# Kernel optimization log

Measured on AMD Instinct MI355X. Metric: run time of the kernel, lower is better.

The kernel has to match this reference:

```python
import jax, jax.numpy as jnp
import numpy as np

HEAD_DIM = 1024
SCALE = HEAD_DIM ** -0.25  # qk_scale defaults to exponent -0.25


def setup_inputs() -> dict:
    key = jax.random.key(0)
    ks = jax.random.split(key, 6)
    B_s, B_q, C = 4096, 4096, 1024
    return {
        "query": jax.random.normal(ks[0], (B_q, C), dtype=jnp.float32),
        "s": jax.random.normal(ks[1], (B_s, C), dtype=jnp.float32),
        "TG_prompt": jax.random.normal(ks[2], (B_s, C), dtype=jnp.float32),
        "W_qkv": jax.random.normal(ks[3], (3 * HEAD_DIM, C), dtype=jnp.float32) * (C ** -0.5),
        "W_proj_s": jax.random.normal(ks[4], (HEAD_DIM, HEAD_DIM), dtype=jnp.float32) * (HEAD_DIM ** -0.5),
        "W_proj_q": jax.random.normal(ks[5], (HEAD_DIM, HEAD_DIM), dtype=jnp.float32) * (HEAD_DIM ** -0.5),
    }


def reference(query, s, TG_prompt, W_qkv, W_proj_s, W_proj_q):
    B_s = s.shape[0]
    t = s + TG_prompt                       # [B_s, C]
    c = jnp.concatenate([t, query], axis=0)  # [B, C], B = B_s + B_q
    x = c @ W_qkv.T                          # [B, 3*head_dim]
    q, k, v = jnp.split(x, 3, axis=-1)       # each [B, head_dim]
    # separate sqrt-scale on q and k, then full [B, B] scores
    attn = jax.nn.softmax((q * SCALE) @ (k.T * SCALE), axis=-1)
    attn_cq = attn[:B_s, B_s:]               # [B_s, B_q]
    attn_qc = attn[B_s:, :B_s]               # [B_q, B_s]
    # matmul against raw query / s (NOT v), then per-branch projection
    x_s = (attn_cq @ query) @ W_proj_s.T     # [B_s, head_dim]
    x_q = (attn_qc @ s) @ W_proj_q.T         # [B_q, head_dim]
    return (x_s, x_q)
```

## Files before the change

kernel.cpp:

```cpp
#include <hip/hip_runtime.h>


typedef unsigned short u16;
typedef __bf16 bf16x8 __attribute__((ext_vector_type(8)));
typedef float f32x4 __attribute__((ext_vector_type(4)));
typedef unsigned short u16x8 __attribute__((ext_vector_type(8)));

#define DEVI static __device__ __forceinline__

DEVI u16 f2b(float f) {
  unsigned int u = __float_as_uint(f);
  u += 0x7fffu + ((u >> 16) & 1u);
  return (u16)(u >> 16);
}

DEVI float exp2_hw(float x) {
  float r;
  asm("v_exp_f32 %0, %1" : "=v"(r) : "v"(x));
  return r;
}

__global__ void prep_all(const float* __restrict__ query, const float* __restrict__ s,
                         const float* __restrict__ tg, const float* __restrict__ w0,
                         const float* __restrict__ w1, const float* __restrict__ w2,
                         u16* __restrict__ cB, u16* __restrict__ sBf,
                         u16* __restrict__ o0, u16* __restrict__ o1,
                         u16* __restrict__ o2, float* __restrict__ rowsum) {
  int b = blockIdx.x;
  if (b >= 6144) {
    int i = (b - 6144) * 1024 + (int)threadIdx.x * 4;
    rowsum[i] = 0.f; rowsum[i + 1] = 0.f; rowsum[i + 2] = 0.f; rowsum[i + 3] = 0.f;
    return;
  }
  if (b < 4096) {
    int base = (b * 256 + threadIdx.x) << 3;
    int row = base >> 10;
    u16x8 o;
    if (row < 4096) {
      float4 a0 = *(const float4*)(s + base);
      float4 a1 = *(const float4*)(s + base + 4);
      float4 b0 = *(const float4*)(tg + base);
      float4 b1 = *(const float4*)(tg + base + 4);
      u16x8 os;
      os[0] = f2b(a0.x); os[1] = f2b(a0.y); os[2] = f2b(a0.z); os[3] = f2b(a0.w);
      os[4] = f2b(a1.x); os[5] = f2b(a1.y); os[6] = f2b(a1.z); os[7] = f2b(a1.w);
      *(u16x8*)(sBf + base) = os;
      o[0] = f2b(a0.x + b0.x); o[1] = f2b(a0.y + b0.y);
      o[2] = f2b(a0.z + b0.z); o[3] = f2b(a0.w + b0.w);
      o[4] = f2b(a1.x + b1.x); o[5] = f2b(a1.y + b1.y);
      o[6] = f2b(a1.z + b1.z); o[7] = f2b(a1.w + b1.w);
    } else {
      int qb = base - 4096 * 1024;
      float4 a0 = *(const float4*)(query + qb);
      float4 a1 = *(const float4*)(query + qb + 4);
      o[0] = f2b(a0.x); o[1] = f2b(a0.y); o[2] = f2b(a0.z); o[3] = f2b(a0.w);
      o[4] = f2b(a1.x); o[5] = f2b(a1.y); o[6] = f2b(a1.z); o[7] = f2b(a1.w);
    }
    *(u16x8*)(cB + base) = o;
  } else {
    const float* in; u16* out; int lb;
    if (b < 5120)      { in = w0; out = o0; lb = b - 4096; }
    else if (b < 5632) { in = w1; out = o1; lb = b - 5120; }
    else               { in = w2; out = o2; lb = b - 5632; }
    int base = (lb * 256 + threadIdx.x) << 3;
    float4 a0 = *(const float4*)(in + base);
    float4 a1 = *(const float4*)(in + base + 4);
    u16x8 o;
    o[0] = f2b(a0.x); o[1] = f2b(a0.y); o[2] = f2b(a0.z); o[3] = f2b(a0.w);
    o[4] = f2b(a1.x); o[5] = f2b(a1.y); o[6] = f2b(a1.z); o[7] = f2b(a1.w);
    *(u16x8*)(out + base) = o;
  }
}

DEVI void kloop(const u16* Ab, const u16* Bb, int lda, int ldb, int K,
                u16* sA, u16* sB, int tid, int wr, int wc, f32x4 (&acc)[4][4]) {
  const int lane = tid & 63;
  const int ar = lane & 15;
  const int sr = tid >> 3;
  const int scL = (tid & 7) << 3;
  const int scG = ((tid & 7) ^ (sr & 7)) << 3;

  const int l7 = lane & 7, l16 = lane >> 4;
  const int p0b = (l16 ^ l7) << 4;
  const int offA0 = (wr + ar) * 128 + p0b;
  const int offB0 = (wc + ar) * 128 + p0b;
  const char* sAc = (const char*)sA;
  const char* sBc = (const char*)sB;

  for (int k0 = 0; k0 < K; k0 += 64) {
#pragma unroll
    for (int it = 0; it < 4; ++it) {
      int r = it * 64 + sr;
      __builtin_amdgcn_global_load_lds(
          (__attribute__((address_space(1))) void*)(Ab + (size_t)r * lda + k0 + scG),
          (__attribute__((address_space(3))) void*)(sA + r * 64 + scL), 16, 0, 0);
    }
#pragma unroll
    for (int it = 0; it < 2; ++it) {
      int r = it * 64 + sr;
      __builtin_amdgcn_global_load_lds(
          (__attribute__((address_space(1))) void*)(Bb + (size_t)r * ldb + k0 + scG),
          (__attribute__((address_space(3))) void*)(sB + r * 64 + scL), 16, 0, 0);
    }
    __syncthreads();
#pragma unroll
    for (int half = 0; half < 2; ++half) {
      const int px = half ? 64 : 0;
      bf16x8 af[4], bfr[4];
#pragma unroll
      for (int t = 0; t < 4; ++t)
        af[t] = *(const bf16x8*)(sAc + ((offA0 ^ px) + t * 2048));
#pragma unroll
      for (int t = 0; t < 4; ++t)
        bfr[t] = *(const bf16x8*)(sBc + ((offB0 ^ px) + t * 2048));
#pragma unroll
      for (int tm = 0; tm < 4; ++tm)
#pragma unroll
        for (int tn = 0; tn < 4; ++tn)
          acc[tm][tn] = __builtin_amdgcn_mfma_f32_16x16x32_bf16(
              af[tm], bfr[tn], acc[tm][tn], 0, 0, 0);
    }
    __syncthreads();
  }
}

DEVI void kloop128(const u16* Ab, const u16* Bb, int lda, int ldb, int K,
                   u16* sA, u16* sB, int tid, int wr, int wc, f32x4 (&acc)[4][4]) {
  const int lane = tid & 63;
  const int ar = lane & 15;
  const int sr = tid >> 3;
  const int scL = (tid & 7) << 3;
  const int scG = ((tid & 7) ^ (sr & 7)) << 3;

  const int l7 = lane & 7, l16 = lane >> 4;
  const int p0b = (l16 ^ l7) << 4;
  const int offA0 = (wr + ar) * 128 + p0b;
  const int offB0 = (wc + ar) * 128 + p0b;
  const char* sAc = (const char*)sA;
  const char* sBc = (const char*)sB;

  for (int k0 = 0; k0 < K; k0 += 64) {
#pragma unroll
    for (int it = 0; it < 4; ++it) {
      int r = it * 32 + sr;
      __builtin_amdgcn_global_load_lds(
          (__attribute__((address_space(1))) void*)(Ab + (size_t)r * lda + k0 + scG),
          (__attribute__((address_space(3))) void*)(sA + r * 64 + scL), 16, 0, 0);
    }
#pragma unroll
    for (int it = 0; it < 4; ++it) {
      int r = it * 32 + sr;
      __builtin_amdgcn_global_load_lds(
          (__attribute__((address_space(1))) void*)(Bb + (size_t)r * ldb + k0 + scG),
          (__attribute__((address_space(3))) void*)(sB + r * 64 + scL), 16, 0, 0);
    }
    __syncthreads();
#pragma unroll
    for (int half = 0; half < 2; ++half) {
      const int px = half ? 64 : 0;
      bf16x8 af[4], bfr[4];
#pragma unroll
      for (int t = 0; t < 4; ++t)
        af[t] = *(const bf16x8*)(sAc + ((offA0 ^ px) + t * 2048));
#pragma unroll
      for (int t = 0; t < 4; ++t)
        bfr[t] = *(const bf16x8*)(sBc + ((offB0 ^ px) + t * 2048));
#pragma unroll
      for (int tm = 0; tm < 4; ++tm)
#pragma unroll
        for (int tn = 0; tn < 4; ++tn)
          acc[tm][tn] = __builtin_amdgcn_mfma_f32_16x16x32_bf16(
              af[tm], bfr[tn], acc[tm][tn], 0, 0, 0);
    }
    __syncthreads();
  }
}

__global__ __launch_bounds__(512)
void gemm_qkv(const u16* __restrict__ cB, const u16* __restrict__ WqkB,
              u16* __restrict__ qks,
              const u16* __restrict__ WpsB, const u16* __restrict__ WpqB,
              const u16* __restrict__ qBf, const u16* __restrict__ sBf,
              u16* __restrict__ VsT, u16* __restrict__ VqT,
              float sq, float sk) {
  __shared__ __align__(16) u16 sA[256 * 64];
  __shared__ __align__(16) u16 sB[128 * 64];
  int b = blockIdx.x;
  b = (b & 7) * 96 + (b >> 3);
  const u16* Ap; const u16* Bp; u16* op;
  int bx, by, ldc;
  bool proj;
  if (b < 512) {
    proj = true;  bx = b & 15; by = b >> 4;
    Ap = cB; Bp = WqkB; op = qks; ldc = 2048;
  } else {
    proj = false;
    int b2 = b - 512;
    int z = b2 >> 7, rem = b2 & 127;
    bx = rem & 31; by = rem >> 5;
    Ap = z ? WpqB : WpsB; Bp = z ? sBf : qBf; op = z ? VqT : VsT; ldc = 4096;
  }
  const int tid = threadIdx.x;
  const int lane = tid & 63;
  const int wave = tid >> 6;
  const int wr = (wave >> 1) * 64;
  const int wc = (wave & 1) * 64;

  f32x4 acc[4][4];
#pragma unroll
  for (int i = 0; i < 4; ++i)
#pragma unroll
    for (int j = 0; j < 4; ++j) acc[i][j] = f32x4{0.f, 0.f, 0.f, 0.f};

  kloop(Ap + (size_t)(by * 256) * 1024, Bp + (size_t)(bx * 128) * 1024,
        1024, 1024, 1024, sA, sB, tid, wr, wc, acc);

  const int qr = (lane >> 4) * 4;
  const int qc = lane & 15;
#pragma unroll
  for (int tm = 0; tm < 4; ++tm)
#pragma unroll
    for (int r = 0; r < 4; ++r) {
      int row = by * 256 + wr + tm * 16 + qr + r;
#pragma unroll
      for (int tn = 0; tn < 4; ++tn) {
        int col = bx * 128 + wc + tn * 16 + qc;
        float sc = proj ? ((col < 1024) ? sq : sk) : 1.0f;
        op[(size_t)row * ldc + col] = f2b(acc[tm][tn][r] * sc);
      }
    }
}

__global__ __launch_bounds__(512)
void gemm_scores(const u16* __restrict__ qks, u16* __restrict__ Pcq,
                 u16* __restrict__ Pqc, float* __restrict__ rowsum) {
  __shared__ __align__(16) u16 sA[256 * 64];
  __shared__ __align__(16) u16 sB[128 * 64];
  const int tid = threadIdx.x;
  const int lane = tid & 63;
  const int wave = tid >> 6;
  const int wr = (wave >> 1) * 64;
  const int wc = (wave & 1) * 64;
  int b = blockIdx.x;
  int swz = (b & 7) * 256 + (b >> 3);
  const int bx = swz & 63;
  const int by = swz >> 6;

  f32x4 acc[4][4];
#pragma unroll
  for (int i = 0; i < 4; ++i)
#pragma unroll
    for (int j = 0; j < 4; ++j) acc[i][j] = f32x4{0.f, 0.f, 0.f, 0.f};

  kloop(qks + (size_t)(by * 256) * 2048,
        qks + 1024 + (size_t)(bx * 128) * 2048,
        2048, 2048, 1024, sA, sB, tid, wr, wc, acc);

  const int qr = (lane >> 4) * 4;
  const int qc = lane & 15;
  const bool top = (by < 16);
  const bool left = (bx < 32);
  u16* pdst = nullptr;
  if (top && !left) pdst = Pcq;
  if (!top && left) pdst = Pqc;
  const int growb = by * 256 + wr;
  const int rbase = growb - (top ? 0 : 4096);
  const int cbase = bx * 128 + wc - (left ? 0 : 4096);
#pragma unroll
  for (int tm = 0; tm < 4; ++tm) {
    float e[4][4];
    float rsum[4] = {0.f, 0.f, 0.f, 0.f};
#pragma unroll
    for (int tn = 0; tn < 4; ++tn)
#pragma unroll
      for (int r = 0; r < 4; ++r) {
        e[tn][r] = exp2_hw(acc[tm][tn][r]);
        rsum[r] += e[tn][r];
      }
#pragma unroll
    for (int r = 0; r < 4; ++r) {
      float v = rsum[r];
      v += __shfl_xor(v, 1);
      v += __shfl_xor(v, 2);
      v += __shfl_xor(v, 4);
      v += __shfl_xor(v, 8);
      if ((lane & 15) == 0)
        atomicAdd(&rowsum[growb + tm * 16 + qr + r], v);
    }
    if (pdst) {
#pragma unroll
      for (int tn = 0; tn < 4; ++tn)
#pragma unroll
        for (int r = 0; r < 4; ++r) {
          int row = rbase + tm * 16 + qr + r;
          pdst[(size_t)row * 4096 + cbase + tn * 16 + qc] = f2b(e[tn][r]);
        }
    }
  }
}

__global__ __launch_bounds__(256)
void gemm_pv(const u16* __restrict__ Pcq, const u16* __restrict__ Pqc,
             const u16* __restrict__ VsT, const u16* __restrict__ VqT,
             const float* __restrict__ rowsum,
             float* __restrict__ out0, float* __restrict__ out1) {
  __shared__ __align__(16) u16 sA[128 * 64];
  __shared__ __align__(16) u16 sB[128 * 64];
  const int tid = threadIdx.x;
  const int lane = tid & 63;
  const int wave = tid >> 6;
  const int wr = (wave >> 1) * 64;
  const int wc = (wave & 1) * 64;
  int b = blockIdx.x;
  int swz = (b & 7) * 64 + (b >> 3);
  const int z = swz >> 8;
  const int rem = swz & 255;
  const int by = rem >> 3;
  const int bx = rem & 7;

  f32x4 acc[4][4];
#pragma unroll
  for (int i = 0; i < 4; ++i)
#pragma unroll
    for (int j = 0; j < 4; ++j) acc[i][j] = f32x4{0.f, 0.f, 0.f, 0.f};

  kloop128((z ? Pqc : Pcq) + (size_t)(by * 128) * 4096,
           (z ? VqT : VsT) + (size_t)(bx * 128) * 4096,
           4096, 4096, 4096, sA, sB, tid, wr, wc, acc);

  const int qr = (lane >> 4) * 4;
  const int qc = lane & 15;
  float* of = z ? out1 : out0;
  const float* rsz = rowsum + z * 4096;
#pragma unroll
  for (int tm = 0; tm < 4; ++tm)
#pragma unroll
    for (int r = 0; r < 4; ++r) {
      int row = by * 128 + wr + tm * 16 + qr + r;
      float inv = 1.0f / rsz[row];
#pragma unroll
      for (int tn = 0; tn < 4; ++tn) {
        int col = bx * 128 + wc + tn * 16 + qc;
        of[(size_t)row * 1024 + col] = acc[tm][tn][r] * inv;
      }
    }
}


extern "C" void kernel_launch(void* const* d_in, const int* in_sizes, int n_in,
                              void* d_out, int out_size, void* d_ws, size_t ws_size,
                              hipStream_t stream) {
  (void)in_sizes; (void)n_in; (void)out_size; (void)ws_size;
  const float* query = (const float*)d_in[0];
  const float* s     = (const float*)d_in[1];
  const float* tg    = (const float*)d_in[2];
  const float* Wqkv  = (const float*)d_in[3];
  const float* Wps   = (const float*)d_in[4];
  const float* Wpq   = (const float*)d_in[5];
  float* out = (float*)d_out;

  char* ws = (char*)d_ws;
  u16* cB     = (u16*)ws; ws += (size_t)8192 * 1024 * 2;
  u16* sBf    = (u16*)ws; ws += (size_t)4096 * 1024 * 2;
  u16* qks    = (u16*)ws; ws += (size_t)8192 * 2048 * 2;
  u16* WqkB   = (u16*)ws; ws += (size_t)2048 * 1024 * 2;
  u16* WpsB   = (u16*)ws; ws += (size_t)1024 * 1024 * 2;
  u16* WpqB   = (u16*)ws; ws += (size_t)1024 * 1024 * 2;
  u16* VsT    = (u16*)ws; ws += (size_t)1024 * 4096 * 2;
  u16* VqT    = (u16*)ws; ws += (size_t)1024 * 4096 * 2;
  u16* Pcq    = (u16*)ws; ws += (size_t)4096 * 4096 * 2;
  u16* Pqc    = (u16*)ws; ws += (size_t)4096 * 4096 * 2;
  float* rowsum = (float*)ws;

  const u16* qBf = cB + (size_t)4096 * 1024;

  const float SCALE = 0.17677669529663687f;
  const float LOG2E = 1.4426950408889634f;

  prep_all<<<6152, 256, 0, stream>>>(query, s, tg, Wqkv, Wps, Wpq,
                                     cB, sBf, WqkB, WpsB, WpqB, rowsum);
  gemm_qkv<<<768, 512, 0, stream>>>(cB, WqkB, qks, WpsB, WpqB, qBf, sBf,
                                    VsT, VqT, SCALE * LOG2E, SCALE);
  gemm_scores<<<2048, 512, 0, stream>>>(qks, Pcq, Pqc, rowsum);
  gemm_pv<<<512, 256, 0, stream>>>(Pcq, Pqc, VsT, VqT, rowsum,
                                   out, out + (size_t)4096 * 1024);
}
```

Measured before the change: 421.1 us.

## Rewrite scores GEMM as 256x256 tile with direct-to-LDS double-buffered pipeline

Replaces the shared kloop in the scores kernel with a dedicated 256x256 tile loop. It uses global_load_lds async copies into swizzled, double-buffered LDS split by k-halves, and interleaves staging of the next tiles with MFMA phases, raising priority around the MFMAs. The larger tile raises arithmetic intensity and the pipeline hides global load latency behind compute. The costs are more accumulator registers (128 floats per lane), more barriers, and a 2D grid that drops the old block swizzle, which may lower L2 locality.

```diff
diff --git a/kernel.cpp b/kernel.cpp
--- a/kernel.cpp
+++ b/kernel.cpp
@@ -232,50 +232,128 @@
 }
 
 __global__ __launch_bounds__(512)
-void gemm_scores(const u16* __restrict__ qks, u16* __restrict__ Pcq,
-                 u16* __restrict__ Pqc, float* __restrict__ rowsum) {
-  __shared__ __align__(16) u16 sA[256 * 64];
-  __shared__ __align__(16) u16 sB[128 * 64];
+void gemm_scores(const u16* __restrict__ A, const u16* __restrict__ B,
+                 u16* __restrict__ Pcq, u16* __restrict__ Pqc,
+                 float* __restrict__ rowsum) {
+  __shared__ __align__(16) u16 lds[2][2][2][256 * 32];
   const int tid = threadIdx.x;
   const int lane = tid & 63;
   const int wave = tid >> 6;
-  const int wr = (wave >> 1) * 64;
-  const int wc = (wave & 1) * 64;
-  int b = blockIdx.x;
-  int swz = (b & 7) * 256 + (b >> 3);
-  const int bx = swz & 63;
-  const int by = swz >> 6;
-
-  f32x4 acc[4][4];
-#pragma unroll
-  for (int i = 0; i < 4; ++i)
+  const int wm = wave >> 2;
+  const int wn = wave & 3;
+  const int bx = blockIdx.x, by = blockIdx.y;
+
+  const int glog = (lane & 3) ^ ((lane >> 2) & 3) ^ ((lane >> 4) & 3);
+  const int srow0 = wave * 32 + (lane >> 2);
+  const int ldsoff = wave * 2048 + lane * 16;
+
+  const int ar = lane & 15, l16 = lane >> 4;
+  const int gread = (l16 ^ (ar & 3) ^ ((ar >> 2) & 3)) << 4;
+  const int offA = (wm * 128 + ar) * 64 + gread;
+  const int offB = (wn * 64 + ar) * 64 + gread;
+
+  const u16* Ag = A + (size_t)(by * 256) * 2048;
+  const u16* Bg = B + (size_t)(bx * 256) * 2048;
+
+#define STG(BUF, MAT, KH, KT, SRC)                                            \
+  _Pragma("unroll")                                                           \
+  for (int j_ = 0; j_ < 2; ++j_) {                                            \
+    __builtin_amdgcn_global_load_lds(                                         \
+        (__attribute__((address_space(1))) void*)((SRC) +                     \
+            (size_t)(srow0 + 16 * j_) * 2048 + (KT) * 64 + (KH) * 32 + glog * 8), \
+        (__attribute__((address_space(3))) void*)((char*)&lds[BUF][MAT][KH][0] + \
+            ldsoff + j_ * 1024), 16, 0, 0);                                   \
+  }
+
+#define RD_A(AQ, KH)                                                          \
+  _Pragma("unroll")                                                           \
+  for (int t_ = 0; t_ < 4; ++t_)                                              \
+    a[t_] = *(const bf16x8*)((const char*)&lds[cur][0][KH][0] + offA +        \
+                             (AQ) * 4096 + t_ * 1024);
+
+#define RD_B(KH)                                                              \
+  _Pragma("unroll")                                                           \
+  for (int t_ = 0; t_ < 4; ++t_)                                              \
+    b[t_] = *(const bf16x8*)((const char*)&lds[cur][1][KH][0] + offB +        \
+                             t_ * 1024);
+
+#define PH_MFMA(AQ)                                                           \
+  __builtin_amdgcn_s_setprio(1);                                              \
+  _Pragma("unroll")                                                           \
+  for (int tm_ = 0; tm_ < 4; ++tm_)                                           \
+    _Pragma("unroll")                                                         \
+    for (int tn_ = 0; tn_ < 4; ++tn_)                                         \
+      acc[(AQ) * 4 + tm_][tn_] = __builtin_amdgcn_mfma_f32_16x16x32_bf16(     \
+          a[tm_], b[tn_], acc[(AQ) * 4 + tm_][tn_], 0, 0, 0);                 \
+  __builtin_amdgcn_s_setprio(0);
+
+#define BAR() __builtin_amdgcn_s_barrier()
+#define LGKM0() asm volatile("s_waitcnt lgkmcnt(0)" ::: "memory")
+
+  f32x4 acc[8][4];
+#pragma unroll
+  for (int i = 0; i < 8; ++i)
 #pragma unroll
     for (int j = 0; j < 4; ++j) acc[i][j] = f32x4{0.f, 0.f, 0.f, 0.f};
 
-  kloop(qks + (size_t)(by * 256) * 2048,
-        qks + 1024 + (size_t)(bx * 128) * 2048,
-        2048, 2048, 1024, sA, sB, tid, wr, wc, acc);
+  STG(0, 0, 0, 0, Ag) STG(0, 1, 0, 0, Bg)
+  STG(0, 0, 1, 0, Ag) STG(0, 1, 1, 0, Bg)
+  STG(1, 0, 0, 1, Ag) STG(1, 1, 0, 1, Bg)
+  asm volatile("s_waitcnt vmcnt(4)" ::: "memory");
+  BAR();
+
+#pragma unroll 1
+  for (int kt = 0; kt < 16; ++kt) {
+    const int cur = kt & 1;
+    bf16x8 a[4], b[4];
+
+    RD_A(0, 0) RD_B(0)
+    if (kt < 15) { STG(cur ^ 1, 0, 1, kt + 1, Ag) }
+    else { asm volatile("s_waitcnt vmcnt(0)" ::: "memory"); }
+    BAR(); LGKM0();
+    PH_MFMA(0)
+    BAR();
+
+    RD_A(1, 0)
+    if (kt < 15) { STG(cur ^ 1, 1, 1, kt + 1, Bg) }
+    BAR(); LGKM0();
+    PH_MFMA(1)
+    BAR();
+
+    RD_A(0, 1) RD_B(1)
+    if (kt < 14) { STG(cur, 0, 0, kt + 2, Ag) }
+    BAR(); LGKM0();
+    PH_MFMA(0)
+    BAR();
+
+    RD_A(1, 1)
+    if (kt < 14) { STG(cur, 1, 0, kt + 2, Bg) }
+    if (kt < 15) { asm volatile("s_waitcnt vmcnt(4)" ::: "memory"); }
+    BAR(); LGKM0();
+    PH_MFMA(1)
+    BAR();
+  }
 
   const int qr = (lane >> 4) * 4;
   const int qc = lane & 15;
   const bool top = (by < 16);
-  const bool left = (bx < 32);
+  const bool left = (bx < 16);
   u16* pdst = nullptr;
   if (top && !left) pdst = Pcq;
   if (!top && left) pdst = Pqc;
-  const int growb = by * 256 + wr;
+  const int growb = by * 256 + wm * 128;
   const int rbase = growb - (top ? 0 : 4096);
-  const int cbase = bx * 128 + wc - (left ? 0 : 4096);
-#pragma unroll
-  for (int tm = 0; tm < 4; ++tm) {
+  const int cbase = bx * 256 + wn * 64 - (left ? 0 : 4096);
+#pragma unroll
+  for (int i = 0; i < 8; ++i) {
     float e[4][4];
     float rsum[4] = {0.f, 0.f, 0.f, 0.f};
 #pragma unroll
-    for (int tn = 0; tn < 4; ++tn)
+    for (int j = 0; j < 4; ++j)
 #pragma unroll
       for (int r = 0; r < 4; ++r) {
-        e[tn][r] = exp2_hw(acc[tm][tn][r]);
-        rsum[r] += e[tn][r];
+        e[j][r] = exp2_hw(acc[i][j][r]);
+        rsum[r] += e[j][r];
       }
 #pragma unroll
     for (int r = 0; r < 4; ++r) {
@@ -285,18 +363,24 @@
       v += __shfl_xor(v, 4);
       v += __shfl_xor(v, 8);
       if ((lane & 15) == 0)
-        atomicAdd(&rowsum[growb + tm * 16 + qr + r], v);
+        atomicAdd(&rowsum[growb + i * 16 + qr + r], v);
     }
     if (pdst) {
 #pragma unroll
-      for (int tn = 0; tn < 4; ++tn)
+      for (int j = 0; j < 4; ++j)
 #pragma unroll
         for (int r = 0; r < 4; ++r) {
-          int row = rbase + tm * 16 + qr + r;
-          pdst[(size_t)row * 4096 + cbase + tn * 16 + qc] = f2b(e[tn][r]);
+          int row = rbase + i * 16 + qr + r;
+          pdst[(size_t)row * 4096 + cbase + j * 16 + qc] = f2b(e[j][r]);
         }
     }
   }
+#undef STG
+#undef RD_A
+#undef RD_B
+#undef PH_MFMA
+#undef BAR
+#undef LGKM0
 }
 
 __global__ __launch_bounds__(256)
@@ -381,7 +465,7 @@
                                      cB, sBf, WqkB, WpsB, WpqB, rowsum);
   gemm_qkv<<<768, 512, 0, stream>>>(cB, WqkB, qks, WpsB, WpqB, qBf, sBf,
                                     VsT, VqT, SCALE * LOG2E, SCALE);
-  gemm_scores<<<2048, 512, 0, stream>>>(qks, Pcq, Pqc, rowsum);
+  gemm_scores<<<dim3(32, 32), 512, 0, stream>>>(qks, qks + 1024, Pcq, Pqc, rowsum);
   gemm_pv<<<512, 256, 0, stream>>>(Pcq, Pqc, VsT, VqT, rowsum,
                                    out, out + (size_t)4096 * 1024);
 }
```

Measured after the change: 447.3 us. +6.2%, slower.

## Enlarge scores GEMM tile to 256x256 with inline LDS-direct swizzled k-loop

Applied to the files above, without the earlier changes.

The scores kernel moves from 256x128 block tiles to 256x256 tiles, with each wave computing 128x64 (8x4 MFMA tiles) instead of 64x64. The shared kloop helper is replaced by an inline loop that uses global_load_lds direct-to-LDS loads with an XOR swizzle, and the grid changes to a 32x32 dim3 without the block-order swizzle. The aim is more operand reuse per loaded byte and fewer blocks. In exchange it uses more registers and LDS per block, lowering occupancy, and the k-loop is single-buffered with no load/compute overlap.

```diff
diff --git a/kernel.cpp b/kernel.cpp
--- a/kernel.cpp
+++ b/kernel.cpp
@@ -235,39 +235,85 @@
 void gemm_scores(const u16* __restrict__ qks, u16* __restrict__ Pcq,
                  u16* __restrict__ Pqc, float* __restrict__ rowsum) {
   __shared__ __align__(16) u16 sA[256 * 64];
-  __shared__ __align__(16) u16 sB[128 * 64];
+  __shared__ __align__(16) u16 sB[256 * 64];
   const int tid = threadIdx.x;
   const int lane = tid & 63;
   const int wave = tid >> 6;
-  const int wr = (wave >> 1) * 64;
-  const int wc = (wave & 1) * 64;
-  int b = blockIdx.x;
-  int swz = (b & 7) * 256 + (b >> 3);
-  const int bx = swz & 63;
-  const int by = swz >> 6;
-
-  f32x4 acc[4][4];
-#pragma unroll
-  for (int i = 0; i < 4; ++i)
+  const int wm = wave >> 2;
+  const int wn = wave & 3;
+  const int wr = wm * 128;
+  const int wc = wn * 64;
+  const int bx = blockIdx.x, by = blockIdx.y;
+
+  const int ar = lane & 15;
+  const int sr = tid >> 3;
+  const int scL = (tid & 7) << 3;
+  const int scG = ((tid & 7) ^ (sr & 7)) << 3;
+
+  const int l7 = lane & 7, l16 = lane >> 4;
+  const int p0b = (l16 ^ l7) << 4;
+  const int offA0 = (wr + ar) * 128 + p0b;
+  const int offB0 = (wc + ar) * 128 + p0b;
+  const char* sAc = (const char*)sA;
+  const char* sBc = (const char*)sB;
+
+  const u16* Ab = qks + (size_t)(by * 256) * 2048;
+  const u16* Bb = qks + 1024 + (size_t)(bx * 256) * 2048;
+
+  f32x4 acc[8][4];
+#pragma unroll
+  for (int i = 0; i < 8; ++i)
 #pragma unroll
     for (int j = 0; j < 4; ++j) acc[i][j] = f32x4{0.f, 0.f, 0.f, 0.f};
 
-  kloop(qks + (size_t)(by * 256) * 2048,
-        qks + 1024 + (size_t)(bx * 128) * 2048,
-        2048, 2048, 1024, sA, sB, tid, wr, wc, acc);
+  for (int k0 = 0; k0 < 1024; k0 += 64) {
+#pragma unroll
+    for (int it = 0; it < 4; ++it) {
+      int r = it * 64 + sr;
+      __builtin_amdgcn_global_load_lds(
+          (__attribute__((address_space(1))) void*)(Ab + (size_t)r * 2048 + k0 + scG),
+          (__attribute__((address_space(3))) void*)(sA + r * 64 + scL), 16, 0, 0);
+    }
+#pragma unroll
+    for (int it = 0; it < 4; ++it) {
+      int r = it * 64 + sr;
+      __builtin_amdgcn_global_load_lds(
+          (__attribute__((address_space(1))) void*)(Bb + (size_t)r * 2048 + k0 + scG),
+          (__attribute__((address_space(3))) void*)(sB + r * 64 + scL), 16, 0, 0);
+    }
+    __syncthreads();
+#pragma unroll
+    for (int half = 0; half < 2; ++half) {
+      const int px = half ? 64 : 0;
+      bf16x8 af[8], bfr[4];
+#pragma unroll
+      for (int t = 0; t < 8; ++t)
+        af[t] = *(const bf16x8*)(sAc + ((offA0 ^ px) + t * 2048));
+#pragma unroll
+      for (int t = 0; t < 4; ++t)
+        bfr[t] = *(const bf16x8*)(sBc + ((offB0 ^ px) + t * 2048));
+#pragma unroll
+      for (int tm = 0; tm < 8; ++tm)
+#pragma unroll
+        for (int tn = 0; tn < 4; ++tn)
+          acc[tm][tn] = __builtin_amdgcn_mfma_f32_16x16x32_bf16(
+              af[tm], bfr[tn], acc[tm][tn], 0, 0, 0);
+    }
+    __syncthreads();
+  }
 
   const int qr = (lane >> 4) * 4;
   const int qc = lane & 15;
   const bool top = (by < 16);
-  const bool left = (bx < 32);
+  const bool left = (bx < 16);
   u16* pdst = nullptr;
   if (top && !left) pdst = Pcq;
   if (!top && left) pdst = Pqc;
   const int growb = by * 256 + wr;
   const int rbase = growb - (top ? 0 : 4096);
-  const int cbase = bx * 128 + wc - (left ? 0 : 4096);
-#pragma unroll
-  for (int tm = 0; tm < 4; ++tm) {
+  const int cbase = bx * 256 + wc - (left ? 0 : 4096);
+#pragma unroll
+  for (int tm = 0; tm < 8; ++tm) {
     float e[4][4];
     float rsum[4] = {0.f, 0.f, 0.f, 0.f};
 #pragma unroll
@@ -381,7 +427,7 @@
                                      cB, sBf, WqkB, WpsB, WpqB, rowsum);
   gemm_qkv<<<768, 512, 0, stream>>>(cB, WqkB, qks, WpsB, WpqB, qBf, sBf,
                                     VsT, VqT, SCALE * LOG2E, SCALE);
-  gemm_scores<<<2048, 512, 0, stream>>>(qks, Pcq, Pqc, rowsum);
+  gemm_scores<<<dim3(32, 32), 512, 0, stream>>>(qks, Pcq, Pqc, rowsum);
   gemm_pv<<<512, 256, 0, stream>>>(Pcq, Pqc, VsT, VqT, rowsum,
                                    out, out + (size_t)4096 * 1024);
 }
```

Result: slower. 451.7 us (+7.3%).

## Split-K the PV GEMM into two halves with a combine-and-normalize kernel

Applied to the files above, without the earlier changes.

The attention-times-values GEMM now splits its 4096-long K dimension into two halves, launching twice as many blocks. Each half writes unnormalized fp32 partials into workspace buffers that are dead by that point. A new elementwise kernel sums the two partials and applies the softmax row-sum division. This raises parallelism on the PV stage at the cost of extra global traffic for the partials and one more launch. The scores GEMM also drops its block-index swizzle in favour of a plain 2D grid, which may change L2 reuse.

```diff
diff --git a/kernel.cpp b/kernel.cpp
--- a/kernel.cpp
+++ b/kernel.cpp
@@ -241,10 +241,8 @@
   const int wave = tid >> 6;
   const int wr = (wave >> 1) * 64;
   const int wc = (wave & 1) * 64;
-  int b = blockIdx.x;
-  int swz = (b & 7) * 256 + (b >> 3);
-  const int bx = swz & 63;
-  const int by = swz >> 6;
+  const int bx = blockIdx.x;
+  const int by = blockIdx.y;
 
   f32x4 acc[4][4];
 #pragma unroll
@@ -302,8 +300,7 @@
 __global__ __launch_bounds__(256)
 void gemm_pv(const u16* __restrict__ Pcq, const u16* __restrict__ Pqc,
              const u16* __restrict__ VsT, const u16* __restrict__ VqT,
-             const float* __restrict__ rowsum,
-             float* __restrict__ out0, float* __restrict__ out1) {
+             float* __restrict__ part0, float* __restrict__ part1) {
   __shared__ __align__(16) u16 sA[128 * 64];
   __shared__ __align__(16) u16 sB[128 * 64];
   const int tid = threadIdx.x;
@@ -312,11 +309,13 @@
   const int wr = (wave >> 1) * 64;
   const int wc = (wave & 1) * 64;
   int b = blockIdx.x;
-  int swz = (b & 7) * 64 + (b >> 3);
+  const int kh = b >> 9;
+  int rem = b & 511;
+  int swz = (rem & 7) * 64 + (rem >> 3);
   const int z = swz >> 8;
-  const int rem = swz & 255;
-  const int by = rem >> 3;
-  const int bx = rem & 7;
+  const int rem2 = swz & 255;
+  const int by = rem2 >> 3;
+  const int bx = rem2 & 7;
 
   f32x4 acc[4][4];
 #pragma unroll
@@ -324,26 +323,40 @@
 #pragma unroll
     for (int j = 0; j < 4; ++j) acc[i][j] = f32x4{0.f, 0.f, 0.f, 0.f};
 
-  kloop128((z ? Pqc : Pcq) + (size_t)(by * 128) * 4096,
-           (z ? VqT : VsT) + (size_t)(bx * 128) * 4096,
-           4096, 4096, 4096, sA, sB, tid, wr, wc, acc);
+  kloop128((z ? Pqc : Pcq) + (size_t)(by * 128) * 4096 + kh * 2048,
+           (z ? VqT : VsT) + (size_t)(bx * 128) * 4096 + kh * 2048,
+           4096, 4096, 2048, sA, sB, tid, wr, wc, acc);
 
   const int qr = (lane >> 4) * 4;
   const int qc = lane & 15;
-  float* of = z ? out1 : out0;
-  const float* rsz = rowsum + z * 4096;
+  float* dst = kh ? part1 : part0;
 #pragma unroll
   for (int tm = 0; tm < 4; ++tm)
 #pragma unroll
     for (int r = 0; r < 4; ++r) {
-      int row = by * 128 + wr + tm * 16 + qr + r;
-      float inv = 1.0f / rsz[row];
+      int row = z * 4096 + by * 128 + wr + tm * 16 + qr + r;
 #pragma unroll
       for (int tn = 0; tn < 4; ++tn) {
         int col = bx * 128 + wc + tn * 16 + qc;
-        of[(size_t)row * 1024 + col] = acc[tm][tn][r] * inv;
+        dst[(size_t)row * 1024 + col] = acc[tm][tn][r];
       }
     }
+}
+
+__global__ __launch_bounds__(256)
+void combine_div(const float* __restrict__ p0, const float* __restrict__ p1,
+                 const float* __restrict__ rowsum, float* __restrict__ out) {
+  size_t i = ((size_t)blockIdx.x * 256 + (size_t)threadIdx.x) * 16;
+  float inv = 1.0f / rowsum[i >> 10];
+#pragma unroll
+  for (int j = 0; j < 16; j += 4) {
+    float4 a = *(const float4*)(p0 + i + j);
+    float4 b = *(const float4*)(p1 + i + j);
+    float4 o;
+    o.x = (a.x + b.x) * inv; o.y = (a.y + b.y) * inv;
+    o.z = (a.z + b.z) * inv; o.w = (a.w + b.w) * inv;
+    *(float4*)(out + i + j) = o;
+  }
 }
 
 
@@ -374,6 +387,9 @@
 
   const u16* qBf = cB + (size_t)4096 * 1024;
 
+  float* part0 = (float*)d_ws;
+  float* part1 = part0 + (size_t)8192 * 1024;
+
   const float SCALE = 0.17677669529663687f;
   const float LOG2E = 1.4426950408889634f;
 
@@ -381,7 +397,7 @@
                                      cB, sBf, WqkB, WpsB, WpqB, rowsum);
   gemm_qkv<<<768, 512, 0, stream>>>(cB, WqkB, qks, WpsB, WpqB, qBf, sBf,
                                     VsT, VqT, SCALE * LOG2E, SCALE);
-  gemm_scores<<<2048, 512, 0, stream>>>(qks, Pcq, Pqc, rowsum);
-  gemm_pv<<<512, 256, 0, stream>>>(Pcq, Pqc, VsT, VqT, rowsum,
-                                   out, out + (size_t)4096 * 1024);
-}
+  gemm_scores<<<dim3(64, 32), 512, 0, stream>>>(qks, Pcq, Pqc, rowsum);
+  gemm_pv<<<1024, 256, 0, stream>>>(Pcq, Pqc, VsT, VqT, part0, part1);
+  combine_div<<<2048, 256, 0, stream>>>(part0, part1, rowsum, out);
+}
```

Measured after the change: 427.8 us. Within noise of the previous version (+1.6%).
